# Optimization experiments

Measured on AMD Instinct MI355X. Metric: run time of the kernel, lower is better.

The kernel has to match this reference:

```python
import jax, jax.numpy as jnp
import numpy as np

WS = 7        # window_size
SHIFT = 3     # shift_size
HEADS = 12
EMBED = 384


def _relative_position_index(ws: int) -> np.ndarray:
    coords = np.stack(np.meshgrid(np.arange(ws), np.arange(ws), indexing='ij'))  # [2,ws,ws]
    flat = coords.reshape(2, -1)                                                 # [2,ws*ws]
    rel = flat[:, :, None] - flat[:, None, :]                                     # [2,N,N]
    rel = rel.transpose(1, 2, 0)
    rel[:, :, 0] += ws - 1
    rel[:, :, 1] += ws - 1
    rel[:, :, 0] *= 2 * ws - 1
    return rel.sum(-1)  # [ws*ws, ws*ws]


def setup_inputs() -> dict:
    key = jax.random.key(0)
    ks = jax.random.split(key, 6)
    B, H, W, C = 32, 56, 56, EMBED
    x = jax.random.normal(ks[0], (B, H * W, C), dtype=jnp.float32)
    s = 0.02
    qkv_w = jax.random.normal(ks[1], (C, 3 * C), dtype=jnp.float32) * s
    qkv_b = jnp.zeros((3 * C,), dtype=jnp.float32)
    proj_w = jax.random.normal(ks[2], (C, C), dtype=jnp.float32) * s
    proj_b = jnp.zeros((C,), dtype=jnp.float32)
    rel_bias_table = jax.random.normal(ks[3], ((2 * WS - 1) ** 2, HEADS), dtype=jnp.float32) * s
    return {"x": x, "qkv_w": qkv_w, "qkv_b": qkv_b, "proj_w": proj_w,
            "proj_b": proj_b, "rel_bias_table": rel_bias_table, "H": H, "W": W}


def reference(x, qkv_w, qkv_b, proj_w, proj_b, rel_bias_table, H, W):
    B, L, C = x.shape
    hd = C // HEADS
    scale = hd ** (-0.5)
    ws = WS
    x = x.reshape(B, H, W, C)
    # pad to multiples of window size (static python ints)
    pad_r = (ws - W % ws) % ws
    pad_b_ = (ws - H % ws) % ws
    if pad_r or pad_b_:
        x = jnp.pad(x, ((0, 0), (0, pad_b_), (0, pad_r), (0, 0)))
    Hp, Wp = H + pad_b_, W + pad_r
    # cyclic shift
    if SHIFT > 0:
        x = jnp.roll(x, shift=(-SHIFT, -SHIFT), axis=(1, 2))
    # window partition -> [nW, ws*ws, C]
    nh, nw = Hp // ws, Wp // ws
    xw = x.reshape(B, nh, ws, nw, ws, C).transpose(0, 1, 3, 2, 4, 5).reshape(-1, ws * ws, C)
    # qkv projection
    qkv = xw @ qkv_w + qkv_b                               # [nW, N, 3C]
    qkv = qkv.reshape(-1, ws * ws, 3, HEADS, hd).transpose(2, 0, 3, 1, 4)
    q, k, v = qkv[0], qkv[1], qkv[2]                        # [nW, heads, N, hd]
    attn = jnp.einsum('whnd,whmd->whnm', q, k) * scale
    rpi = jnp.asarray(_relative_position_index(ws))         # [N, N] static
    bias = rel_bias_table[rpi.reshape(-1)].reshape(ws * ws, ws * ws, HEADS)
    attn = attn + bias.transpose(2, 0, 1)[None]             # [1, heads, N, N]
    attn = jax.nn.softmax(attn, axis=-1)
    out = jnp.einsum('whnm,whmd->whnd', attn, v)            # [nW, heads, N, hd]
    out = out.transpose(0, 2, 1, 3).reshape(-1, ws, ws, C)
    # merge windows
    out = out.reshape(B, nh, nw, ws, ws, C).transpose(0, 1, 3, 2, 4, 5).reshape(B, Hp, Wp, C)
    if SHIFT > 0:
        out = jnp.roll(out, shift=(SHIFT, SHIFT), axis=(1, 2))
    if pad_r or pad_b_:
        out = out[:, :H, :W, :]
    out = out.reshape(B, H * W, C)
    return out @ proj_w + proj_b
```

## Files before the change

kernel.cpp:

```cpp
#include <hip/hip_runtime.h>


typedef __attribute__((ext_vector_type(8))) short short8;
typedef __attribute__((ext_vector_type(4))) float floatx4;

#define CDIM  384
#define QKVN  1152
#define MROWS 100352
#define LROW  3136

static constexpr size_t QKV_ELEMS = 38535168ull;
static constexpr size_t OFF_Q    = 0;
static constexpr size_t OFF_K    = OFF_Q  + QKV_ELEMS * 2 + 4096;
static constexpr size_t OFF_V    = OFF_K  + QKV_ELEMS * 2 + 4096;
static constexpr size_t OFF_AO   = OFF_V  + QKV_ELEMS * 2 + 4096;
static constexpr size_t OFF_WQ   = OFF_AO + (size_t)MROWS * CDIM * 2 + 4096;
static constexpr size_t OFF_WP   = OFF_WQ + (size_t)QKVN * CDIM * 2 + 256;
static constexpr size_t OFF_BIAS = OFF_WP + (size_t)CDIM * CDIM * 2 + 256;
static constexpr size_t OFF_LUT  = OFF_BIAS + (size_t)12 * 64 * 64 * 4 + 256;

__device__ __forceinline__ unsigned short f2bf(float f) {
  unsigned int u = __float_as_uint(f);
  unsigned int lsb = (u >> 16) & 1u;
  u += 0x7fffu + lsb;
  return (unsigned short)(u >> 16);
}

__device__ __forceinline__ void gl2lds16(const void* g, void* l) {
  __builtin_amdgcn_global_load_lds(
      (const __attribute__((address_space(1))) unsigned int*)g,
      (__attribute__((address_space(3))) unsigned int*)l, 16, 0, 0);
}

__global__ __launch_bounds__(256) void prep_kernel(
    const float* __restrict__ x, const float* __restrict__ qkv_w,
    const float* __restrict__ proj_w, const float* __restrict__ rbt,
    char* __restrict__ ws) {
  unsigned short* Wq = (unsigned short*)(ws + OFF_WQ);
  unsigned short* Wp = (unsigned short*)(ws + OFF_WP);
  unsigned short* XB = (unsigned short*)(ws + OFF_AO);
  float* biasp = (float*)(ws + OFF_BIAS);
  int* lut = (int*)(ws + OFF_LUT);
  const int tid = blockIdx.x * blockDim.x + threadIdx.x;
  const int stride = gridDim.x * blockDim.x;
  for (int idx = tid; idx < QKVN * CDIM; idx += stride) {
    int n = idx / CDIM, k = idx - n * CDIM;
    Wq[idx] = f2bf(qkv_w[(size_t)k * QKVN + n]);
  }
  for (int idx = tid; idx < CDIM * CDIM; idx += stride) {
    int n = idx / CDIM, k = idx - n * CDIM;
    Wp[idx] = f2bf(proj_w[(size_t)k * CDIM + n]);
  }
  for (int idx = tid; idx < 12 * 64 * 64; idx += stride) {
    int h = idx / 4096;
    int rem = idx - h * 4096;
    int lane = rem / 64;
    int e = rem - lane * 64;
    int fm = e >> 4, fn = (e >> 2) & 3, r = e & 3;
    int row = fm * 16 + (lane >> 4) * 4 + r;
    int col = fn * 16 + (lane & 15);
    float v = -1e30f;
    if (row < 49 && col < 49) {
      int i = row / 7, j = row - i * 7;
      int k2 = col / 7, l2 = col - k2 * 7;
      int rpi = (i - k2 + 6) * 13 + (j - l2 + 6);
      v = rbt[rpi * 12 + h];
    }
    biasp[idx] = v;
  }
  for (int idx = tid; idx < MROWS; idx += stride) {
    int b_ = idx / LROW, l = idx - b_ * LROW;
    int y = l / 56, xx = l - y * 56;
    int yr = y + 53; if (yr >= 56) yr -= 56;
    int xr = xx + 53; if (xr >= 56) xr -= 56;
    int win = b_ * 64 + (yr / 7) * 8 + (xr / 7);
    int nidx = (yr % 7) * 7 + (xr % 7);
    lut[idx] = win * 18816 + nidx * 32;
  }
  const size_t n8 = (size_t)MROWS * CDIM / 8;
  for (size_t idx = tid; idx < n8; idx += stride) {
    const float4* s = (const float4*)(x + idx * 8);
    float4 f0 = s[0], f1 = s[1];
    uint4 o;
    o.x = (unsigned)f2bf(f0.x) | ((unsigned)f2bf(f0.y) << 16);
    o.y = (unsigned)f2bf(f0.z) | ((unsigned)f2bf(f0.w) << 16);
    o.z = (unsigned)f2bf(f1.x) | ((unsigned)f2bf(f1.y) << 16);
    o.w = (unsigned)f2bf(f1.z) | ((unsigned)f2bf(f1.w) << 16);
    ((uint4*)XB)[idx] = o;
  }
}

__global__ __launch_bounds__(256) void qkv_gemm(
    const float* __restrict__ qkv_b, char* __restrict__ ws) {
  __shared__ unsigned short As[2][128][32];
  __shared__ unsigned short Bs[2][128][32];
  const unsigned short* XB = (const unsigned short*)(ws + OFF_AO);
  const unsigned short* Wq = (const unsigned short*)(ws + OFF_WQ);
  unsigned short* Qb = (unsigned short*)(ws + OFF_Q);
  unsigned short* Kb = (unsigned short*)(ws + OFF_K);
  unsigned short* Vb = (unsigned short*)(ws + OFF_V);
  const int* lut = (const int*)(ws + OFF_LUT);
  const int L = blockIdx.x;
  const int xcd = L & 7, slot = L >> 3;
  const int g9 = slot / 9;
  const int m0 = (g9 * 8 + xcd) * 128;
  const int n0 = (slot - g9 * 9) * 128;
  const int t = threadIdx.x;
  const int lane = t & 63, li = lane & 15, qd = lane >> 4;
  const int wv = t >> 6, wm = wv >> 1, wn = wv & 1;
  const int ld_r = lane >> 2;
  const int ld_c = (lane & 3) * 8;
  const unsigned short* agp = XB + (size_t)(m0 + wv * 32 + ld_r) * CDIM + ld_c;
  const unsigned short* bgp = Wq + (size_t)(n0 + wv * 32 + ld_r) * CDIM + ld_c;

#define QSTAGE(buf, k0)                                          \
  do {                                                           \
    gl2lds16(agp + (k0),             &As[buf][wv * 32][0]);      \
    gl2lds16(agp + (k0) + 16 * CDIM, &As[buf][wv * 32 + 16][0]); \
    gl2lds16(bgp + (k0),             &Bs[buf][wv * 32][0]);      \
    gl2lds16(bgp + (k0) + 16 * CDIM, &Bs[buf][wv * 32 + 16][0]); \
  } while (0)

  floatx4 acc[4][4] = {};
  QSTAGE(0, 0);
  __syncthreads();
  for (int kt = 0; kt < 12; ++kt) {
    const int cur = kt & 1;
    if (kt < 11) QSTAGE(cur ^ 1, (kt + 1) * 32);
    short8 a[4], b[4];
#pragma unroll
    for (int f = 0; f < 4; f++)
      a[f] = *(const short8*)&As[cur][wm * 64 + f * 16 + li][qd * 8];
#pragma unroll
    for (int f = 0; f < 4; f++)
      b[f] = *(const short8*)&Bs[cur][wn * 64 + f * 16 + li][qd * 8];
#pragma unroll
    for (int i = 0; i < 4; i++)
#pragma unroll
      for (int j = 0; j < 4; j++)
        acc[i][j] = __builtin_amdgcn_mfma_f32_16x16x32_bf16(a[i], b[j], acc[i][j], 0, 0, 0);
    __syncthreads();
  }
#undef QSTAGE

  const int which = n0 / CDIM;
  unsigned short* dst = which == 0 ? Qb : (which == 1 ? Kb : Vb);
  const float mul = (which == 0) ? 0.17677669529663689f : 1.0f;
#pragma unroll
  for (int i = 0; i < 4; i++) {
    int lbase[4];
#pragma unroll
    for (int r = 0; r < 4; r++)
      lbase[r] = lut[m0 + wm * 64 + i * 16 + qd * 4 + r];
#pragma unroll
    for (int j = 0; j < 4; j++) {
      int c = n0 + wn * 64 + j * 16 + li;
      int cc = c - which * CDIM;
      int head = cc >> 5, d = cc & 31;
      int hd_off = head * 1568 + d;
      float bval = qkv_b[c];
#pragma unroll
      for (int r = 0; r < 4; r++) {
        size_t off = (size_t)(lbase[r] + hd_off);
        dst[off] = f2bf((acc[i][j][r] + bval) * mul);
      }
    }
  }
}

__global__ __launch_bounds__(256) void attn_kernel(char* __restrict__ ws) {
  __shared__ unsigned short SMEM[4][64 * 72];
  const int win = blockIdx.x;
  const int t = threadIdx.x, wv = t >> 6, lane = t & 63;
  const int h = blockIdx.y * 4 + wv;
  const int li = lane & 15, qd = lane >> 4;
  unsigned short* Sm = &SMEM[wv][0];
  const size_t whoff = (size_t)(win * 12 + h) * 49 * 32;
  const unsigned short* Qb = (const unsigned short*)(ws + OFF_Q) + whoff;
  const unsigned short* Kb = (const unsigned short*)(ws + OFF_K) + whoff;
  const unsigned short* Vb = (const unsigned short*)(ws + OFF_V) + whoff;
  const float* biasp = (const float*)(ws + OFF_BIAS) + ((size_t)h * 64 + lane) * 64;

  {
    const uint2* vsrc = (const uint2*)Vb;
    for (int idx = lane; idx < 392; idx += 64) {
      uint2 d = vsrc[idx];
      unsigned short* p = Sm + (idx >> 3) * 34 + (idx & 7) * 4;
      *(unsigned int*)p = d.x;
      *(unsigned int*)(p + 2) = d.y;
    }
    for (int idx = lane; idx < 120; idx += 64) {
      unsigned short* p = Sm + (49 + (idx >> 3)) * 34 + (idx & 7) * 4;
      *(unsigned int*)p = 0;
      *(unsigned int*)(p + 2) = 0;
    }
  }

  short8 qa[4], kb4[4];
#pragma unroll
  for (int f = 0; f < 4; f++) {
    qa[f] = *(const short8*)(Qb + (f * 16 + li) * 32 + qd * 8);
    kb4[f] = *(const short8*)(Kb + (f * 16 + li) * 32 + qd * 8);
  }
  floatx4 s[4][4] = {};
#pragma unroll
  for (int i = 0; i < 4; i++)
#pragma unroll
    for (int j = 0; j < 4; j++)
      s[i][j] = __builtin_amdgcn_mfma_f32_16x16x32_bf16(qa[i], kb4[j], s[i][j], 0, 0, 0);

  short8 vb[2][2];
#pragma unroll
  for (int ss = 0; ss < 2; ss++)
#pragma unroll
    for (int nf = 0; nf < 2; nf++) {
      short8 tmp;
#pragma unroll
      for (int j = 0; j < 8; j++)
        tmp[j] = (short)Sm[(ss * 32 + qd * 8 + j) * 34 + nf * 16 + li];
      vb[ss][nf] = tmp;
    }

  float rsum[4][4];
#pragma unroll
  for (int fm = 0; fm < 4; fm++) {
#pragma unroll
    for (int fn = 0; fn < 4; fn++) {
      floatx4 bv = *(const floatx4*)(biasp + (fm * 4 + fn) * 4);
#pragma unroll
      for (int r = 0; r < 4; r++)
        s[fm][fn][r] = __expf(s[fm][fn][r] + bv[r]);
    }
#pragma unroll
    for (int r = 0; r < 4; r++) {
      float v = s[fm][0][r] + s[fm][1][r] + s[fm][2][r] + s[fm][3][r];
      v += __shfl_xor(v, 1);
      v += __shfl_xor(v, 2);
      v += __shfl_xor(v, 4);
      v += __shfl_xor(v, 8);
      rsum[fm][r] = v;
    }
#pragma unroll
    for (int fn = 0; fn < 4; fn++)
#pragma unroll
      for (int r = 0; r < 4; r++)
        Sm[(fm * 16 + qd * 4 + r) * 72 + fn * 16 + li] = f2bf(s[fm][fn][r]);
  }

  floatx4 o[4][2] = {};
#pragma unroll
  for (int fm = 0; fm < 4; fm++)
#pragma unroll
    for (int ss = 0; ss < 2; ss++) {
      short8 pa = *(const short8*)&Sm[(fm * 16 + li) * 72 + ss * 32 + qd * 8];
#pragma unroll
      for (int nf = 0; nf < 2; nf++)
        o[fm][nf] = __builtin_amdgcn_mfma_f32_16x16x32_bf16(pa, vb[ss][nf], o[fm][nf], 0, 0, 0);
    }

  unsigned short* AO = (unsigned short*)(ws + OFF_AO);
  const int b_ = win >> 6, wrem = win & 63, wy = wrem >> 3, wx = wrem & 7;
#pragma unroll
  for (int fm = 0; fm < 4; fm++)
#pragma unroll
    for (int r = 0; r < 4; r++) {
      int n = fm * 16 + qd * 4 + r;
      if (n >= 49) continue;
      float inv = 1.0f / rsum[fm][r];
      int i_ = n / 7, j_ = n - i_ * 7;
      int y = wy * 7 + i_ + 3;  if (y >= 56) y -= 56;
      int xx = wx * 7 + j_ + 3; if (xx >= 56) xx -= 56;
      size_t base = ((size_t)b_ * LROW + y * 56 + xx) * CDIM + h * 32;
#pragma unroll
      for (int nf = 0; nf < 2; nf++)
        AO[base + nf * 16 + li] = f2bf(o[fm][nf][r] * inv);
    }
}

__global__ __launch_bounds__(256) void proj_gemm(
    const float* __restrict__ proj_b, char* __restrict__ ws,
    float* __restrict__ out) {
  __shared__ unsigned short As[2][128][32];
  __shared__ unsigned short Bs[2][128][32];
  const unsigned short* AO = (const unsigned short*)(ws + OFF_AO);
  const unsigned short* Wp = (const unsigned short*)(ws + OFF_WP);
  const int L = blockIdx.x;
  const int xcd = L & 7, slot = L >> 3;
  const int g3 = slot / 3;
  const int m0 = (g3 * 8 + xcd) * 128;
  const int n0 = (slot - g3 * 3) * 128;
  const int t = threadIdx.x;
  const int lane = t & 63, li = lane & 15, qd = lane >> 4;
  const int wv = t >> 6, wm = wv >> 1, wn = wv & 1;
  const int ld_r = lane >> 2;
  const int ld_c = (lane & 3) * 8;
  const unsigned short* agp = AO + (size_t)(m0 + wv * 32 + ld_r) * CDIM + ld_c;
  const unsigned short* bgp = Wp + (size_t)(n0 + wv * 32 + ld_r) * CDIM + ld_c;

#define PSTAGE(buf, k0)                                          \
  do {                                                           \
    gl2lds16(agp + (k0),             &As[buf][wv * 32][0]);      \
    gl2lds16(agp + (k0) + 16 * CDIM, &As[buf][wv * 32 + 16][0]); \
    gl2lds16(bgp + (k0),             &Bs[buf][wv * 32][0]);      \
    gl2lds16(bgp + (k0) + 16 * CDIM, &Bs[buf][wv * 32 + 16][0]); \
  } while (0)

  floatx4 acc[4][4] = {};
  PSTAGE(0, 0);
  __syncthreads();
  for (int kt = 0; kt < 12; ++kt) {
    const int cur = kt & 1;
    if (kt < 11) PSTAGE(cur ^ 1, (kt + 1) * 32);
    short8 a[4], b[4];
#pragma unroll
    for (int f = 0; f < 4; f++)
      a[f] = *(const short8*)&As[cur][wm * 64 + f * 16 + li][qd * 8];
#pragma unroll
    for (int f = 0; f < 4; f++)
      b[f] = *(const short8*)&Bs[cur][wn * 64 + f * 16 + li][qd * 8];
#pragma unroll
    for (int i = 0; i < 4; i++)
#pragma unroll
      for (int j = 0; j < 4; j++)
        acc[i][j] = __builtin_amdgcn_mfma_f32_16x16x32_bf16(a[i], b[j], acc[i][j], 0, 0, 0);
    __syncthreads();
  }
#undef PSTAGE

#pragma unroll
  for (int i = 0; i < 4; i++)
#pragma unroll
    for (int j = 0; j < 4; j++) {
      int c = n0 + wn * 64 + j * 16 + li;
      float bv = proj_b[c];
#pragma unroll
      for (int r = 0; r < 4; r++) {
        int m = m0 + wm * 64 + i * 16 + qd * 4 + r;
        out[(size_t)m * CDIM + c] = acc[i][j][r] + bv;
      }
    }
}

extern "C" void kernel_launch(void* const* d_in, const int* in_sizes, int n_in,
                              void* d_out, int out_size, void* d_ws, size_t ws_size,
                              hipStream_t stream) {
  const float* x      = (const float*)d_in[0];
  const float* qkv_w  = (const float*)d_in[1];
  const float* qkv_b  = (const float*)d_in[2];
  const float* proj_w = (const float*)d_in[3];
  const float* proj_b = (const float*)d_in[4];
  const float* rbt    = (const float*)d_in[5];
  char* ws = (char*)d_ws;
  float* out = (float*)d_out;

  prep_kernel<<<2048, 256, 0, stream>>>(x, qkv_w, proj_w, rbt, ws);
  qkv_gemm<<<7056, 256, 0, stream>>>(qkv_b, ws);
  attn_kernel<<<dim3(2048, 3), 256, 0, stream>>>(ws);
  proj_gemm<<<2352, 256, 0, stream>>>(proj_b, ws, out);
}
```

Baseline: 615.2 us.

## Double block M-tile to 256 with 512 threads and prefetch two stages ahead in GEMMs

Both GEMM kernels now run 8 waves per block over a 256-row A tile that shares a single 128-column B tile, which halves B traffic per output. The k-loop becomes a two-deep prefetch: each stage is issued two iterations ahead, with explicit vmcnt waits and raw s_barrier in place of __syncthreads. The aim is to overlap global-to-LDS loads with MFMA work and cut redundant weight loads. Risks include exact vmcnt counting, since each wave now issues 3 loads per stage, and the epilogue's wm/wn indexing for 8 waves. That indexing is not shown and may not be updated.

```diff
diff --git a/kernel.cpp b/kernel.cpp
--- a/kernel.cpp
+++ b/kernel.cpp
@@ -31,6 +31,18 @@
       (const __attribute__((address_space(1))) unsigned int*)g,
       (__attribute__((address_space(3))) unsigned int*)l, 16, 0, 0);
 }
+
+#define RAW_BARRIER()                           \
+  do {                                          \
+    __builtin_amdgcn_sched_barrier(0);          \
+    asm volatile("s_barrier" ::: "memory");     \
+    __builtin_amdgcn_sched_barrier(0);          \
+  } while (0)
+#define WAIT_VM(N)                                        \
+  do {                                                    \
+    asm volatile("s_waitcnt vmcnt(" #N ")" ::: "memory"); \
+    __builtin_amdgcn_sched_barrier(0);                    \
+  } while (0)
 
 __global__ __launch_bounds__(256) void prep_kernel(
     const float* __restrict__ x, const float* __restrict__ qkv_w,
@@ -90,9 +102,9 @@
   }
 }
 
-__global__ __launch_bounds__(256) void qkv_gemm(
+__global__ __launch_bounds__(512, 6) void qkv_gemm(
     const float* __restrict__ qkv_b, char* __restrict__ ws) {
-  __shared__ unsigned short As[2][128][32];
+  __shared__ unsigned short As[2][256][32];
   __shared__ unsigned short Bs[2][128][32];
   const unsigned short* XB = (const unsigned short*)(ws + OFF_AO);
   const unsigned short* Wq = (const unsigned short*)(ws + OFF_WQ);
@@ -103,30 +115,32 @@
   const int L = blockIdx.x;
   const int xcd = L & 7, slot = L >> 3;
   const int g9 = slot / 9;
-  const int m0 = (g9 * 8 + xcd) * 128;
+  const int m0 = (g9 * 8 + xcd) * 256;
   const int n0 = (slot - g9 * 9) * 128;
   const int t = threadIdx.x;
   const int lane = t & 63, li = lane & 15, qd = lane >> 4;
-  const int wv = t >> 6, wm = wv >> 1, wn = wv & 1;
+  const int wv = t >> 6;
+  const int wm = wv >> 1, wn = wv & 1;
   const int ld_r = lane >> 2;
   const int ld_c = (lane & 3) * 8;
   const unsigned short* agp = XB + (size_t)(m0 + wv * 32 + ld_r) * CDIM + ld_c;
-  const unsigned short* bgp = Wq + (size_t)(n0 + wv * 32 + ld_r) * CDIM + ld_c;
+  const unsigned short* bgp = Wq + (size_t)(n0 + wv * 16 + ld_r) * CDIM + ld_c;
 
 #define QSTAGE(buf, k0)                                          \
   do {                                                           \
     gl2lds16(agp + (k0),             &As[buf][wv * 32][0]);      \
     gl2lds16(agp + (k0) + 16 * CDIM, &As[buf][wv * 32 + 16][0]); \
-    gl2lds16(bgp + (k0),             &Bs[buf][wv * 32][0]);      \
-    gl2lds16(bgp + (k0) + 16 * CDIM, &Bs[buf][wv * 32 + 16][0]); \
+    gl2lds16(bgp + (k0),             &Bs[buf][wv * 16][0]);      \
   } while (0)
 
   floatx4 acc[4][4] = {};
   QSTAGE(0, 0);
-  __syncthreads();
+  QSTAGE(1, 32);
   for (int kt = 0; kt < 12; ++kt) {
     const int cur = kt & 1;
-    if (kt < 11) QSTAGE(cur ^ 1, (kt + 1) * 32);
+    if (kt < 11) { WAIT_VM(3); }
+    else         { WAIT_VM(0); }
+    RAW_BARRIER();
     short8 a[4], b[4];
 #pragma unroll
     for (int f = 0; f < 4; f++)
@@ -139,7 +153,8 @@
 #pragma unroll
       for (int j = 0; j < 4; j++)
         acc[i][j] = __builtin_amdgcn_mfma_f32_16x16x32_bf16(a[i], b[j], acc[i][j], 0, 0, 0);
-    __syncthreads();
+    RAW_BARRIER();
+    if (kt + 2 < 12) QSTAGE(cur, (kt + 2) * 32);
   }
 #undef QSTAGE
 
@@ -277,40 +292,42 @@
     }
 }
 
-__global__ __launch_bounds__(256) void proj_gemm(
+__global__ __launch_bounds__(512, 6) void proj_gemm(
     const float* __restrict__ proj_b, char* __restrict__ ws,
     float* __restrict__ out) {
-  __shared__ unsigned short As[2][128][32];
+  __shared__ unsigned short As[2][256][32];
   __shared__ unsigned short Bs[2][128][32];
   const unsigned short* AO = (const unsigned short*)(ws + OFF_AO);
   const unsigned short* Wp = (const unsigned short*)(ws + OFF_WP);
   const int L = blockIdx.x;
   const int xcd = L & 7, slot = L >> 3;
   const int g3 = slot / 3;
-  const int m0 = (g3 * 8 + xcd) * 128;
+  const int m0 = (g3 * 8 + xcd) * 256;
   const int n0 = (slot - g3 * 3) * 128;
   const int t = threadIdx.x;
   const int lane = t & 63, li = lane & 15, qd = lane >> 4;
-  const int wv = t >> 6, wm = wv >> 1, wn = wv & 1;
+  const int wv = t >> 6;
+  const int wm = wv >> 1, wn = wv & 1;
   const int ld_r = lane >> 2;
   const int ld_c = (lane & 3) * 8;
   const unsigned short* agp = AO + (size_t)(m0 + wv * 32 + ld_r) * CDIM + ld_c;
-  const unsigned short* bgp = Wp + (size_t)(n0 + wv * 32 + ld_r) * CDIM + ld_c;
+  const unsigned short* bgp = Wp + (size_t)(n0 + wv * 16 + ld_r) * CDIM + ld_c;
 
 #define PSTAGE(buf, k0)                                          \
   do {                                                           \
     gl2lds16(agp + (k0),             &As[buf][wv * 32][0]);      \
     gl2lds16(agp + (k0) + 16 * CDIM, &As[buf][wv * 32 + 16][0]); \
-    gl2lds16(bgp + (k0),             &Bs[buf][wv * 32][0]);      \
-    gl2lds16(bgp + (k0) + 16 * CDIM, &Bs[buf][wv * 32 + 16][0]); \
+    gl2lds16(bgp + (k0),             &Bs[buf][wv * 16][0]);      \
   } while (0)
 
   floatx4 acc[4][4] = {};
   PSTAGE(0, 0);
-  __syncthreads();
+  PSTAGE(1, 32);
   for (int kt = 0; kt < 12; ++kt) {
     const int cur = kt & 1;
-    if (kt < 11) PSTAGE(cur ^ 1, (kt + 1) * 32);
+    if (kt < 11) { WAIT_VM(3); }
+    else         { WAIT_VM(0); }
+    RAW_BARRIER();
     short8 a[4], b[4];
 #pragma unroll
     for (int f = 0; f < 4; f++)
@@ -323,7 +340,8 @@
 #pragma unroll
       for (int j = 0; j < 4; j++)
         acc[i][j] = __builtin_amdgcn_mfma_f32_16x16x32_bf16(a[i], b[j], acc[i][j], 0, 0, 0);
-    __syncthreads();
+    RAW_BARRIER();
+    if (kt + 2 < 12) PSTAGE(cur, (kt + 2) * 32);
   }
 #undef PSTAGE
 
@@ -354,7 +372,7 @@
   float* out = (float*)d_out;
 
   prep_kernel<<<2048, 256, 0, stream>>>(x, qkv_w, proj_w, rbt, ws);
-  qkv_gemm<<<7056, 256, 0, stream>>>(qkv_b, ws);
+  qkv_gemm<<<3528, 512, 0, stream>>>(qkv_b, ws);
   attn_kernel<<<dim3(2048, 3), 256, 0, stream>>>(ws);
-  proj_gemm<<<2352, 256, 0, stream>>>(proj_b, ws, out);
-}
+  proj_gemm<<<1176, 512, 0, stream>>>(proj_b, ws, out);
+}
```

Measured after the change: 1.180 ms. 1.92x slower.

## Pipeline GEMM LDS loads with explicit vmcnt waits and transpose V in LDS

Applied to the files above, without the earlier changes.

Both GEMM kernels (QKV and proj) now prefetch two K-tiles up front. Each iteration waits on a partial vmcnt with raw s_barrier instead of __syncthreads, so the next tile's global-to-LDS loads stay in flight during the MFMAs. In the attention kernel, V is stored transposed in LDS so the B-operand fragment can be read as one 16-byte vector load rather than eight scalar loads. The Q/K register loads are also issued before the V staging to overlap latency. The risks are correctness of the hand-written waitcnt accounting and scalar LDS stores with possible bank conflicts during the transpose.

```diff
diff --git a/kernel.cpp b/kernel.cpp
--- a/kernel.cpp
+++ b/kernel.cpp
@@ -31,6 +31,18 @@
       (const __attribute__((address_space(1))) unsigned int*)g,
       (__attribute__((address_space(3))) unsigned int*)l, 16, 0, 0);
 }
+
+#define RAW_BARRIER()                           \
+  do {                                          \
+    __builtin_amdgcn_sched_barrier(0);          \
+    asm volatile("s_barrier" ::: "memory");     \
+    __builtin_amdgcn_sched_barrier(0);          \
+  } while (0)
+#define WAIT_VM(N)                                        \
+  do {                                                    \
+    asm volatile("s_waitcnt vmcnt(" #N ")" ::: "memory"); \
+    __builtin_amdgcn_sched_barrier(0);                    \
+  } while (0)
 
 __global__ __launch_bounds__(256) void prep_kernel(
     const float* __restrict__ x, const float* __restrict__ qkv_w,
@@ -123,10 +135,12 @@
 
   floatx4 acc[4][4] = {};
   QSTAGE(0, 0);
-  __syncthreads();
+  QSTAGE(1, 32);
   for (int kt = 0; kt < 12; ++kt) {
     const int cur = kt & 1;
-    if (kt < 11) QSTAGE(cur ^ 1, (kt + 1) * 32);
+    if (kt < 11) { WAIT_VM(4); }
+    else         { WAIT_VM(0); }
+    RAW_BARRIER();
     short8 a[4], b[4];
 #pragma unroll
     for (int f = 0; f < 4; f++)
@@ -139,7 +153,8 @@
 #pragma unroll
       for (int j = 0; j < 4; j++)
         acc[i][j] = __builtin_amdgcn_mfma_f32_16x16x32_bf16(a[i], b[j], acc[i][j], 0, 0, 0);
-    __syncthreads();
+    RAW_BARRIER();
+    if (kt + 2 < 12) QSTAGE(cur, (kt + 2) * 32);
   }
 #undef QSTAGE
 
@@ -181,27 +196,28 @@
   const unsigned short* Vb = (const unsigned short*)(ws + OFF_V) + whoff;
   const float* biasp = (const float*)(ws + OFF_BIAS) + ((size_t)h * 64 + lane) * 64;
 
+  short8 qa[4], kb4[4];
+#pragma unroll
+  for (int f = 0; f < 4; f++) {
+    qa[f] = *(const short8*)(Qb + (f * 16 + li) * 32 + qd * 8);
+    kb4[f] = *(const short8*)(Kb + (f * 16 + li) * 32 + qd * 8);
+  }
+
+  for (int idx = lane; idx < 512; idx += 64) {
+    Sm[(idx >> 4) * 72 + 48 + (idx & 15)] = 0;
+  }
   {
     const uint2* vsrc = (const uint2*)Vb;
     for (int idx = lane; idx < 392; idx += 64) {
-      uint2 d = vsrc[idx];
-      unsigned short* p = Sm + (idx >> 3) * 34 + (idx & 7) * 4;
-      *(unsigned int*)p = d.x;
-      *(unsigned int*)(p + 2) = d.y;
-    }
-    for (int idx = lane; idx < 120; idx += 64) {
-      unsigned short* p = Sm + (49 + (idx >> 3)) * 34 + (idx & 7) * 4;
-      *(unsigned int*)p = 0;
-      *(unsigned int*)(p + 2) = 0;
-    }
-  }
-
-  short8 qa[4], kb4[4];
-#pragma unroll
-  for (int f = 0; f < 4; f++) {
-    qa[f] = *(const short8*)(Qb + (f * 16 + li) * 32 + qd * 8);
-    kb4[f] = *(const short8*)(Kb + (f * 16 + li) * 32 + qd * 8);
-  }
+      uint2 dv = vsrc[idx];
+      int row = idx >> 3, d0 = (idx & 7) * 4;
+      Sm[(d0 + 0) * 72 + row] = (unsigned short)(dv.x & 0xffff);
+      Sm[(d0 + 1) * 72 + row] = (unsigned short)(dv.x >> 16);
+      Sm[(d0 + 2) * 72 + row] = (unsigned short)(dv.y & 0xffff);
+      Sm[(d0 + 3) * 72 + row] = (unsigned short)(dv.y >> 16);
+    }
+  }
+
   floatx4 s[4][4] = {};
 #pragma unroll
   for (int i = 0; i < 4; i++)
@@ -213,13 +229,8 @@
 #pragma unroll
   for (int ss = 0; ss < 2; ss++)
 #pragma unroll
-    for (int nf = 0; nf < 2; nf++) {
-      short8 tmp;
-#pragma unroll
-      for (int j = 0; j < 8; j++)
-        tmp[j] = (short)Sm[(ss * 32 + qd * 8 + j) * 34 + nf * 16 + li];
-      vb[ss][nf] = tmp;
-    }
+    for (int nf = 0; nf < 2; nf++)
+      vb[ss][nf] = *(const short8*)&Sm[(nf * 16 + li) * 72 + ss * 32 + qd * 8];
 
   float rsum[4][4];
 #pragma unroll
@@ -307,10 +318,12 @@
 
   floatx4 acc[4][4] = {};
   PSTAGE(0, 0);
-  __syncthreads();
+  PSTAGE(1, 32);
   for (int kt = 0; kt < 12; ++kt) {
     const int cur = kt & 1;
-    if (kt < 11) PSTAGE(cur ^ 1, (kt + 1) * 32);
+    if (kt < 11) { WAIT_VM(4); }
+    else         { WAIT_VM(0); }
+    RAW_BARRIER();
     short8 a[4], b[4];
 #pragma unroll
     for (int f = 0; f < 4; f++)
@@ -323,7 +336,8 @@
 #pragma unroll
       for (int j = 0; j < 4; j++)
         acc[i][j] = __builtin_amdgcn_mfma_f32_16x16x32_bf16(a[i], b[j], acc[i][j], 0, 0, 0);
-    __syncthreads();
+    RAW_BARRIER();
+    if (kt + 2 < 12) PSTAGE(cur, (kt + 2) * 32);
   }
 #undef PSTAGE
 
```

Result: no change. 613.4 us (-0.3%).
